# Kernel optimization log

Hardware: AMD Instinct MI355X
Metric: run time of the kernel (lower is better)

The kernel has to match this reference:

```python
import jax, jax.numpy as jnp
import numpy as np


def _init(key, shape, fan_in):
    return jax.random.normal(key, shape, jnp.float32) * (1.0 / np.sqrt(fan_in))


def setup_inputs() -> dict:
    key = jax.random.key(0)
    ks = jax.random.split(key, 12)
    b, n, vd, ad, sd, hd = 32, 2048, 512, 128, 128, 64
    return {
        'vfeat': jax.random.normal(ks[0], (b, n, vd), jnp.float32),
        'afeat': jax.random.normal(ks[1], (b, n, ad), jnp.float32),
        'vfc_w': _init(ks[2], (ad, vd), vd), 'vfc_b': jnp.zeros((ad,), jnp.float32),
        'afc_w': _init(ks[3], (ad, ad), ad), 'afc_b': jnp.zeros((ad,), jnp.float32),
        'am_v_w': _init(ks[4], (sd, sd), sd), 'am_v_b': jnp.zeros((sd,), jnp.float32),
        'am_a_w': _init(ks[5], (sd, sd), sd), 'am_a_b': jnp.zeros((sd,), jnp.float32),
        'am_o_w': _init(ks[6], (1, sd), sd), 'am_o_b': jnp.zeros((1,), jnp.float32),
        'V_w': _init(ks[7], (hd, sd), sd), 'V_b': jnp.zeros((hd,), jnp.float32),
        'W_w': _init(ks[8], (1, hd), hd), 'W_b': jnp.zeros((1,), jnp.float32),
        'cls_w': _init(ks[9], (2, sd), sd), 'cls_b': jnp.zeros((2,), jnp.float32),
    }


def reference(vfeat, afeat, vfc_w, vfc_b, afc_w, afc_b,
              am_v_w, am_v_b, am_a_w, am_a_b, am_o_w, am_o_b,
              V_w, V_b, W_w, W_b, cls_w, cls_b):
    relu = jax.nn.relu
    # vfc / afc projections (dropout is identity in eval mode)
    vo1 = relu(jnp.einsum('bnd,kd->bnk', vfeat, vfc_w) + vfc_b)  # (b,n,128)
    ax = relu(jnp.einsum('bnd,kd->bnk', afeat, afc_w) + afc_b)   # (b,n,128)
    # AM(128): additive gated cross-modal attention: out = sigmoid(Wo tanh(Wv v + Wa a)) * a
    h = jnp.tanh(jnp.einsum('bnk,jk->bnj', vo1, am_v_w) + am_v_b
                 + jnp.einsum('bnk,jk->bnj', ax, am_a_w) + am_a_b)
    att = jax.nn.sigmoid(jnp.einsum('bnj,oj->bno', h, am_o_w) + am_o_b)  # (b,n,1)
    ffeat = att * ax + vo1  # attfeat + vo1, (b,n,128)
    # NOTE: original uses self.V for BOTH f_v and f_u (source bug kept)
    f_v = relu(jnp.einsum('bnk,hk->bnh', ffeat, V_w) + V_b)  # (b,n,64)
    f_u = f_v
    # W is affine with no nonlinearity on (fv_i + fu_j), so
    # W(fv_i + fu_j) = w.fv_i + w.fu_j + b  -- exact rank-1 decomposition
    s_v = f_v @ W_w[0]  # (b,n)
    s_u = f_u @ W_w[0]  # (b,n)
    pair = s_v[:, :, None] + s_u[:, None, :] + W_b[0]  # (b,n_i,n_j)
    p = jax.nn.softmax(pair, axis=1)  # F.softmax(scores, 0) per bag: over i
    scores = p.mean(axis=2)  # mean over j -> (b,n)
    # eval mode: training-only softmax over dim 2 skipped
    zfeat = jnp.einsum('bn,bnk->bk', scores, ffeat)  # (b,128)
    logits = zfeat @ cls_w.T + cls_b  # (b,2)
    return scores, logits
```

## Files before the change

kernel.cpp:

```cpp
#include <hip/hip_runtime.h>
#include <cstddef>
#include <cstdint>


typedef __attribute__((ext_vector_type(8))) short short8;
typedef __attribute__((ext_vector_type(4))) float float4v;

#define MFMA16(a, b, c) __builtin_amdgcn_mfma_f32_16x16x32_bf16((a), (b), (c), 0, 0, 0)

__device__ __forceinline__ unsigned short f2bf(float f) {
    union { float f; unsigned u; } v; v.f = f;
    unsigned r = (v.u + 0x7fffu + ((v.u >> 16) & 1u)) >> 16;
    return (unsigned short)r;
}
__device__ __forceinline__ float bf2f(unsigned short h) {
    union { unsigned u; float f; } v; v.u = ((unsigned)h) << 16;
    return v.f;
}
__device__ __forceinline__ float bf2f_s(short h) { return bf2f((unsigned short)h); }

__device__ __forceinline__ void bfsplit(float x, short& h, short& l) {
    union { float f; unsigned u; } v; v.f = x;
    h = (short)(v.u >> 16);
    union { unsigned u; float f; } hv; hv.u = v.u & 0xffff0000u;
    union { float f; unsigned u; } lv; lv.f = x - hv.f;
    l = (short)(lv.u >> 16);
}

__device__ __forceinline__ float tanh_fast(float x) {
    float e = __builtin_exp2f(x * 2.885390081777927f);
    return 1.f - 2.f / (e + 1.f);
}
__device__ __forceinline__ float sigmoid_fast(float x) {
    return 1.f / (1.f + __builtin_exp2f(-x * 1.4426950408889634f));
}

__device__ __forceinline__ void gload_lds16(const void* g, void* l) {
#if __has_builtin(__builtin_amdgcn_global_load_lds)
    __builtin_amdgcn_global_load_lds(
        (const __attribute__((address_space(1))) unsigned int*)g,
        (__attribute__((address_space(3))) unsigned int*)l, 16, 0, 0);
#else
    *(uint4*)l = *(const uint4*)g;
#endif
}

__global__ __launch_bounds__(256)
void prep(const float* __restrict__ vfc_w, const float* __restrict__ afc_w,
          const float* __restrict__ am_v_w, const float* __restrict__ am_a_w,
          const float* __restrict__ V_w,
          unsigned short* __restrict__ W1h, unsigned short* __restrict__ W1l,
          unsigned short* __restrict__ W1bh, unsigned short* __restrict__ W1bl,
          unsigned short* __restrict__ W2v, unsigned short* __restrict__ W2a,
          unsigned short* __restrict__ W3)
{
    int t = blockIdx.x * 256 + threadIdx.x;
    if (t < 65536) {
        int j = t & 7, lane = (t >> 3) & 63, ks = (t >> 9) & 15, nf = (t >> 13) & 7;
        int n = (lane & 15) + 16 * nf, k = ks * 32 + (lane >> 4) * 8 + j;
        float x = vfc_w[n * 512 + k];
        unsigned short h = f2bf(x);
        W1h[t] = h; W1l[t] = f2bf(x - bf2f(h));
    } else if (t < 81920) {
        int u = t - 65536;
        int j = u & 7, lane = (u >> 3) & 63, ks = (u >> 9) & 3, nf = (u >> 11) & 7;
        int n = (lane & 15) + 16 * nf, k = ks * 32 + (lane >> 4) * 8 + j;
        float x = afc_w[n * 128 + k];
        unsigned short h = f2bf(x);
        W1bh[u] = h; W1bl[u] = f2bf(x - bf2f(h));
    } else if (t < 98304) {
        int u = t - 81920;
        int j = u & 7, lane = (u >> 3) & 63, ks = (u >> 9) & 3, nf = (u >> 11) & 7;
        int n = (lane & 15) + 16 * nf, k = ks * 32 + (lane >> 4) * 8 + j;
        W2v[u] = f2bf(am_v_w[n * 128 + k]);
    } else if (t < 114688) {
        int u = t - 98304;
        int j = u & 7, lane = (u >> 3) & 63, ks = (u >> 9) & 3, nf = (u >> 11) & 7;
        int n = (lane & 15) + 16 * nf, k = ks * 32 + (lane >> 4) * 8 + j;
        W2a[u] = f2bf(am_a_w[n * 128 + k]);
    } else if (t < 122880) {
        int u = t - 114688;
        int j = u & 7, lane = (u >> 3) & 63, ks = (u >> 9) & 3, nf = (u >> 11) & 3;
        int n = (lane & 15) + 16 * nf, k = ks * 32 + (lane >> 4) * 8 + j;
        W3[u] = f2bf(V_w[n * 128 + k]);
    }
}

__global__ __launch_bounds__(256, 3)
void milA(const float* __restrict__ vfeat, const float* __restrict__ afeat,
          const float* __restrict__ vfc_b, const float* __restrict__ afc_b,
          const float* __restrict__ am_v_b, const float* __restrict__ am_a_b,
          const float* __restrict__ am_o_w, const float* __restrict__ am_o_b,
          const float* __restrict__ V_b, const float* __restrict__ W_w,
          const unsigned short* __restrict__ W1h, const unsigned short* __restrict__ W1l,
          const unsigned short* __restrict__ W1bh, const unsigned short* __restrict__ W1bl,
          const unsigned short* __restrict__ W2v, const unsigned short* __restrict__ W2a,
          const unsigned short* __restrict__ W3,
          float* __restrict__ ffeat_out, float* __restrict__ s_out)
{
    __shared__ __align__(16) unsigned short vo1s[8192];
    __shared__ __align__(16) unsigned short axs[8192];
    __shared__ __align__(16) unsigned short bstage[8192];

    const int tid = threadIdx.x;
    const int lane = tid & 63, wid = tid >> 6;
    const int lr = lane & 15, lg = lane >> 4;
    const int row0 = blockIdx.x * 64 + wid * 16;

    float4v acc1[8];
#pragma unroll
    for (int nf = 0; nf < 8; ++nf)
#pragma unroll
        for (int i = 0; i < 4; ++i) acc1[nf][i] = 0.f;

    {
        const float* ap = vfeat + (size_t)(row0 + lr) * 512 + lg * 8;
        float4 a0[2], a1[2], a2[2];
        a0[0] = *(const float4*)(ap);      a0[1] = *(const float4*)(ap + 4);
        a1[0] = *(const float4*)(ap + 32); a1[1] = *(const float4*)(ap + 36);

        for (int ks = 0; ks < 16; ++ks) {
            __syncthreads();
#pragma unroll
            for (int i = 0; i < 4; ++i) {
                const int idx = wid * 4 + i;
                const unsigned short* src = (idx < 8)
                    ? W1h + (size_t)(idx * 16 + ks) * 512
                    : W1l + (size_t)((idx - 8) * 16 + ks) * 512;
                gload_lds16(src + (size_t)lane * 8, &bstage[idx * 512 + lane * 8]);
            }
            __syncthreads();

            if (ks < 14) {
                a2[0] = *(const float4*)(ap + (ks + 2) * 32);
                a2[1] = *(const float4*)(ap + (ks + 2) * 32 + 4);
            }
            short8 ah, al;
            {
                const float xs[8] = {a0[0].x, a0[0].y, a0[0].z, a0[0].w,
                                     a0[1].x, a0[1].y, a0[1].z, a0[1].w};
#pragma unroll
                for (int j = 0; j < 8; ++j) {
                    short h, l; bfsplit(xs[j], h, l);
                    ah[j] = h; al[j] = l;
                }
            }
#pragma unroll
            for (int nf = 0; nf < 8; ++nf) {
                const short8 bh = *(const short8*)&bstage[nf * 512 + lane * 8];
                const short8 bl = *(const short8*)&bstage[4096 + nf * 512 + lane * 8];
                acc1[nf] = MFMA16(ah, bh, acc1[nf]);
                acc1[nf] = MFMA16(ah, bl, acc1[nf]);
                acc1[nf] = MFMA16(al, bh, acc1[nf]);
            }
            a0[0] = a1[0]; a0[1] = a1[1];
            a1[0] = a2[0]; a1[1] = a2[1];
        }
    }
#pragma unroll
    for (int nf = 0; nf < 8; ++nf) {
        const float bb = vfc_b[lr + 16 * nf];
#pragma unroll
        for (int r = 0; r < 4; ++r) {
            float v = fmaxf(acc1[nf][r] + bb, 0.f);
            acc1[nf][r] = v;
            const int row = lg * 4 + r;
            const int col = lr + 16 * nf;
            vo1s[wid * 2048 + row * 128 + (col ^ ((row & 7) << 3))] = f2bf(v);
        }
    }

    float4v acc1b[8];
#pragma unroll
    for (int nf = 0; nf < 8; ++nf)
#pragma unroll
        for (int i = 0; i < 4; ++i) acc1b[nf][i] = 0.f;

    {
        const float* ap = afeat + (size_t)(row0 + lr) * 128 + lg * 8;
        float4 a0[2], a1[2], a2[2];
        a0[0] = *(const float4*)(ap);      a0[1] = *(const float4*)(ap + 4);
        a1[0] = *(const float4*)(ap + 32); a1[1] = *(const float4*)(ap + 36);

        for (int ks = 0; ks < 4; ++ks) {
            __syncthreads();
#pragma unroll
            for (int i = 0; i < 4; ++i) {
                const int idx = wid * 4 + i;
                const unsigned short* src = (idx < 8)
                    ? W1bh + (size_t)(idx * 4 + ks) * 512
                    : W1bl + (size_t)((idx - 8) * 4 + ks) * 512;
                gload_lds16(src + (size_t)lane * 8, &bstage[idx * 512 + lane * 8]);
            }
            __syncthreads();

            if (ks < 2) {
                a2[0] = *(const float4*)(ap + (ks + 2) * 32);
                a2[1] = *(const float4*)(ap + (ks + 2) * 32 + 4);
            }
            short8 ah, al;
            {
                const float xs[8] = {a0[0].x, a0[0].y, a0[0].z, a0[0].w,
                                     a0[1].x, a0[1].y, a0[1].z, a0[1].w};
#pragma unroll
                for (int j = 0; j < 8; ++j) {
                    short h, l; bfsplit(xs[j], h, l);
                    ah[j] = h; al[j] = l;
                }
            }
#pragma unroll
            for (int nf = 0; nf < 8; ++nf) {
                const short8 bh = *(const short8*)&bstage[nf * 512 + lane * 8];
                const short8 bl = *(const short8*)&bstage[4096 + nf * 512 + lane * 8];
                acc1b[nf] = MFMA16(ah, bh, acc1b[nf]);
                acc1b[nf] = MFMA16(ah, bl, acc1b[nf]);
                acc1b[nf] = MFMA16(al, bh, acc1b[nf]);
            }
            a0[0] = a1[0]; a0[1] = a1[1];
            a1[0] = a2[0]; a1[1] = a2[1];
        }
    }
#pragma unroll
    for (int nf = 0; nf < 8; ++nf) {
        const float bb = afc_b[lr + 16 * nf];
#pragma unroll
        for (int r = 0; r < 4; ++r) {
            float v = fmaxf(acc1b[nf][r] + bb, 0.f);
            acc1b[nf][r] = v;
            const int row = lg * 4 + r;
            const int col = lr + 16 * nf;
            axs[wid * 2048 + row * 128 + (col ^ ((row & 7) << 3))] = f2bf(v);
        }
    }

    float4v acc2[8];
#pragma unroll
    for (int nf = 0; nf < 8; ++nf)
#pragma unroll
        for (int i = 0; i < 4; ++i) acc2[nf][i] = 0.f;

    for (int ks = 0; ks < 4; ++ks) {
        __syncthreads();
#pragma unroll
        for (int i = 0; i < 4; ++i) {
            const int idx = wid * 4 + i;
            const unsigned short* src = (idx < 8)
                ? W2v + (size_t)(idx * 4 + ks) * 512
                : W2a + (size_t)((idx - 8) * 4 + ks) * 512;
            gload_lds16(src + (size_t)lane * 8, &bstage[idx * 512 + lane * 8]);
        }
        __syncthreads();
        const int rdoff = (ks * 32 + lg * 8) ^ ((lr & 7) << 3);
        const short8 a2v = *(const short8*)&vo1s[wid * 2048 + lr * 128 + rdoff];
        const short8 a2a = *(const short8*)&axs[wid * 2048 + lr * 128 + rdoff];
#pragma unroll
        for (int nf = 0; nf < 8; ++nf) {
            const short8 bv = *(const short8*)&bstage[nf * 512 + lane * 8];
            const short8 ba = *(const short8*)&bstage[4096 + nf * 512 + lane * 8];
            acc2[nf] = MFMA16(a2v, bv, acc2[nf]);
            acc2[nf] = MFMA16(a2a, ba, acc2[nf]);
        }
    }

    __syncthreads();
#pragma unroll
    for (int i = 0; i < 4; ++i) {
        const int idx = wid * 4 + i;
        gload_lds16(W3 + (size_t)idx * 512 + lane * 8, &bstage[idx * 512 + lane * 8]);
    }

    float attc[4];
    {
        float bias2[8], wo[8];
#pragma unroll
        for (int nf = 0; nf < 8; ++nf) {
            const int c = lr + 16 * nf;
            bias2[nf] = am_v_b[c] + am_a_b[c];
            wo[nf] = am_o_w[c];
        }
        const float ob = am_o_b[0];
#pragma unroll
        for (int r = 0; r < 4; ++r) {
            float p = 0.f;
#pragma unroll
            for (int nf = 0; nf < 8; ++nf)
                p += tanh_fast(acc2[nf][r] + bias2[nf]) * wo[nf];
            p += __shfl_xor(p, 1);
            p += __shfl_xor(p, 2);
            p += __shfl_xor(p, 4);
            p += __shfl_xor(p, 8);
            attc[r] = sigmoid_fast(p + ob);
        }
    }

#pragma unroll
    for (int nf = 0; nf < 8; ++nf)
#pragma unroll
        for (int r = 0; r < 4; ++r)
            ffeat_out[(size_t)(row0 + lg * 4 + r) * 128 + lr + 16 * nf] =
                attc[r] * acc1b[nf][r] + acc1[nf][r];

    float attv;
    {
        const int srcl = (lr >> 2) << 4;
        const float b0 = __shfl(attc[0], srcl);
        const float b1 = __shfl(attc[1], srcl);
        const float b2 = __shfl(attc[2], srcl);
        const float b3 = __shfl(attc[3], srcl);
        attv = (lr & 2) ? ((lr & 1) ? b3 : b2) : ((lr & 1) ? b1 : b0);
    }

    __syncthreads();

    float4v acc3[4];
#pragma unroll
    for (int nf = 0; nf < 4; ++nf)
#pragma unroll
        for (int i = 0; i < 4; ++i) acc3[nf][i] = 0.f;

#pragma unroll
    for (int ks = 0; ks < 4; ++ks) {
        const int rdoff = (ks * 32 + lg * 8) ^ ((lr & 7) << 3);
        const short8 x8 = *(const short8*)&axs[wid * 2048 + lr * 128 + rdoff];
        const short8 v8 = *(const short8*)&vo1s[wid * 2048 + lr * 128 + rdoff];
        short8 a3;
#pragma unroll
        for (int j = 0; j < 8; ++j) {
            float f = attv * bf2f_s(x8[j]) + bf2f_s(v8[j]);
            a3[j] = (short)f2bf(f);
        }
#pragma unroll
        for (int nf = 0; nf < 4; ++nf) {
            const short8 b = *(const short8*)&bstage[(nf * 4 + ks) * 512 + lane * 8];
            acc3[nf] = MFMA16(a3, b, acc3[nf]);
        }
    }

    {
        float vb3[4], ww3[4];
#pragma unroll
        for (int nf = 0; nf < 4; ++nf) {
            const int c = lr + 16 * nf;
            vb3[nf] = V_b[c];
            ww3[nf] = W_w[c];
        }
#pragma unroll
        for (int r = 0; r < 4; ++r) {
            float q = 0.f;
#pragma unroll
            for (int nf = 0; nf < 4; ++nf)
                q += fmaxf(acc3[nf][r] + vb3[nf], 0.f) * ww3[nf];
            q += __shfl_xor(q, 1);
            q += __shfl_xor(q, 2);
            q += __shfl_xor(q, 4);
            q += __shfl_xor(q, 8);
            if (lr == 0) s_out[row0 + lg * 4 + r] = q;
        }
    }
}

__device__ __forceinline__ float wred_sum(float v) {
#pragma unroll
    for (int m = 32; m >= 1; m >>= 1) v += __shfl_xor(v, m);
    return v;
}
__device__ __forceinline__ float wred_max(float v) {
#pragma unroll
    for (int m = 32; m >= 1; m >>= 1) v = fmaxf(v, __shfl_xor(v, m));
    return v;
}

__global__ __launch_bounds__(256)
void milB1(const float* __restrict__ s_in, float* __restrict__ scores_out)
{
    __shared__ float red[4];
    const int t = threadIdx.x, b = blockIdx.x, w = t >> 6;
    const float* sb = s_in + (size_t)b * 2048;

    float v[8];
#pragma unroll
    for (int q = 0; q < 8; ++q) v[q] = sb[q * 256 + t];
    float m = v[0];
#pragma unroll
    for (int q = 1; q < 8; ++q) m = fmaxf(m, v[q]);
    m = wred_max(m);
    if ((t & 63) == 0) red[w] = m;
    __syncthreads();
    const float bm = fmaxf(fmaxf(red[0], red[1]), fmaxf(red[2], red[3]));

    float e[8], sum = 0.f;
#pragma unroll
    for (int q = 0; q < 8; ++q) { e[q] = expf(v[q] - bm); sum += e[q]; }
    sum = wred_sum(sum);
    __syncthreads();
    if ((t & 63) == 0) red[w] = sum;
    __syncthreads();
    const float inv = 1.f / (red[0] + red[1] + red[2] + red[3]);
#pragma unroll
    for (int q = 0; q < 8; ++q)
        scores_out[(size_t)b * 2048 + q * 256 + t] = e[q] * inv;
}

__global__ __launch_bounds__(256)
void milB2(const float* __restrict__ scores, const float* __restrict__ ffeat,
           float* __restrict__ parts)
{
    __shared__ float sh[256];
    __shared__ float zbuf[256];
    const int t = threadIdx.x;
    const int b = blockIdx.x >> 3, part = blockIdx.x & 7;
    const int col = t & 127, half = t >> 7;

    sh[t] = scores[(size_t)b * 2048 + part * 256 + t];
    __syncthreads();

    const float* fb = ffeat + ((size_t)(b * 2048 + part * 256 + half * 128)) * 128 + col;
    const float* sp = sh + half * 128;
    float z = 0.f;
#pragma unroll 8
    for (int nn = 0; nn < 128; ++nn) z += sp[nn] * fb[(size_t)nn * 128];
    zbuf[t] = z;
    __syncthreads();
    if (t < 128) parts[((size_t)(b * 8 + part)) * 128 + t] = zbuf[t] + zbuf[t + 128];
}

__global__ __launch_bounds__(128)
void milB3(const float* __restrict__ parts, const float* __restrict__ cls_w,
           const float* __restrict__ cls_b, float* __restrict__ logits)
{
    __shared__ float zfs[128];
    const int t = threadIdx.x, b = blockIdx.x;
    float zf = 0.f;
#pragma unroll
    for (int p = 0; p < 8; ++p) zf += parts[((size_t)(b * 8 + p)) * 128 + t];
    zfs[t] = zf;
    __syncthreads();
    const int o = t >> 6, c = t & 63;
    float q = zfs[c] * cls_w[o * 128 + c] + zfs[c + 64] * cls_w[o * 128 + c + 64];
    q = wred_sum(q);
    if (c == 0) logits[b * 2 + o] = q + cls_b[o];
}

extern "C" void kernel_launch(void* const* d_in, const int* in_sizes, int n_in,
                              void* d_out, int out_size, void* d_ws, size_t ws_size,
                              hipStream_t stream)
{
    (void)in_sizes; (void)n_in; (void)out_size; (void)ws_size;
    const float* vfeat  = (const float*)d_in[0];
    const float* afeat  = (const float*)d_in[1];
    const float* vfc_w  = (const float*)d_in[2];
    const float* vfc_b  = (const float*)d_in[3];
    const float* afc_w  = (const float*)d_in[4];
    const float* afc_b  = (const float*)d_in[5];
    const float* am_v_w = (const float*)d_in[6];
    const float* am_v_b = (const float*)d_in[7];
    const float* am_a_w = (const float*)d_in[8];
    const float* am_a_b = (const float*)d_in[9];
    const float* am_o_w = (const float*)d_in[10];
    const float* am_o_b = (const float*)d_in[11];
    const float* V_w    = (const float*)d_in[12];
    const float* V_b    = (const float*)d_in[13];
    const float* W_w    = (const float*)d_in[14];
    const float* cls_w  = (const float*)d_in[16];
    const float* cls_b  = (const float*)d_in[17];

    float* scores = (float*)d_out;
    float* logits = (float*)d_out + 32 * 2048;

    char* ws = (char*)d_ws;
    float* ffeat_ws = (float*)ws;
    float* s_ws     = (float*)(ws + 33554432);
    float* parts_ws = (float*)(ws + 33816576);
    unsigned short* W1h  = (unsigned short*)(ws + 33947648);
    unsigned short* W1l  = W1h + 65536;
    unsigned short* W1bh = W1l + 65536;
    unsigned short* W1bl = W1bh + 16384;
    unsigned short* W2v  = W1bl + 16384;
    unsigned short* W2a  = W2v + 16384;
    unsigned short* W3   = W2a + 16384;

    prep<<<480, 256, 0, stream>>>(vfc_w, afc_w, am_v_w, am_a_w, V_w,
                                  W1h, W1l, W1bh, W1bl, W2v, W2a, W3);
    milA<<<1024, 256, 0, stream>>>(vfeat, afeat, vfc_b, afc_b, am_v_b, am_a_b,
                                   am_o_w, am_o_b, V_b, W_w,
                                   W1h, W1l, W1bh, W1bl, W2v, W2a, W3,
                                   ffeat_ws, s_ws);
    milB1<<<32, 256, 0, stream>>>(s_ws, scores);
    milB2<<<256, 256, 0, stream>>>(scores, ffeat_ws, parts_ws);
    milB3<<<32, 128, 0, stream>>>(parts_ws, cls_w, cls_b, logits);
}
```

Baseline: 88.82 us.

## Stage two K-slices of weights per barrier pair and prefetch afeat early

Doubles the shared-memory weight staging buffer so each sync round loads two K-steps of the weight tiles, halving the number of barrier pairs in the vfc, afc and AM GEMM loops. The activation prefetch now covers a 64-wide K chunk, and the first afeat chunk is loaded during the last vfeat step so the afc stage starts without waiting on it. LDS use grows and launch bounds drop from 3 to 2 blocks per SM, which cuts occupancy available for hiding latency.

New measurement: 84.81 us. -4.5%, faster.

```diff
diff --git a/kernel.cpp b/kernel.cpp
--- a/kernel.cpp
+++ b/kernel.cpp
@@ -86,7 +86,7 @@
     }
 }
 
-__global__ __launch_bounds__(256, 3)
+__global__ __launch_bounds__(256, 2)
 void milA(const float* __restrict__ vfeat, const float* __restrict__ afeat,
           const float* __restrict__ vfc_b, const float* __restrict__ afc_b,
           const float* __restrict__ am_v_b, const float* __restrict__ am_a_b,
@@ -98,47 +98,58 @@
           const unsigned short* __restrict__ W3,
           float* __restrict__ ffeat_out, float* __restrict__ s_out)
 {
+    __shared__ __align__(16) unsigned short bstage[16384];
     __shared__ __align__(16) unsigned short vo1s[8192];
     __shared__ __align__(16) unsigned short axs[8192];
-    __shared__ __align__(16) unsigned short bstage[8192];
 
     const int tid = threadIdx.x;
     const int lane = tid & 63, wid = tid >> 6;
     const int lr = lane & 15, lg = lane >> 4;
     const int row0 = blockIdx.x * 64 + wid * 16;
 
+    const float* ap  = vfeat + (size_t)(row0 + lr) * 512 + lg * 8;
+    const float* apb = afeat + (size_t)(row0 + lr) * 128 + lg * 8;
+
     float4v acc1[8];
 #pragma unroll
     for (int nf = 0; nf < 8; ++nf)
 #pragma unroll
         for (int i = 0; i < 4; ++i) acc1[nf][i] = 0.f;
 
-    {
-        const float* ap = vfeat + (size_t)(row0 + lr) * 512 + lg * 8;
-        float4 a0[2], a1[2], a2[2];
-        a0[0] = *(const float4*)(ap);      a0[1] = *(const float4*)(ap + 4);
-        a1[0] = *(const float4*)(ap + 32); a1[1] = *(const float4*)(ap + 36);
-
-        for (int ks = 0; ks < 16; ++ks) {
-            __syncthreads();
-#pragma unroll
-            for (int i = 0; i < 4; ++i) {
-                const int idx = wid * 4 + i;
-                const unsigned short* src = (idx < 8)
-                    ? W1h + (size_t)(idx * 16 + ks) * 512
-                    : W1l + (size_t)((idx - 8) * 16 + ks) * 512;
-                gload_lds16(src + (size_t)lane * 8, &bstage[idx * 512 + lane * 8]);
-            }
-            __syncthreads();
-
-            if (ks < 14) {
-                a2[0] = *(const float4*)(ap + (ks + 2) * 32);
-                a2[1] = *(const float4*)(ap + (ks + 2) * 32 + 4);
-            }
+    float4 acur[4], anxt[4];
+#pragma unroll
+    for (int q = 0; q < 4; ++q)
+        acur[q] = *(const float4*)(ap + (q >> 1) * 32 + (q & 1) * 4);
+
+    for (int s = 0; s < 8; ++s) {
+        __syncthreads();
+#pragma unroll
+        for (int i = 0; i < 8; ++i) {
+            const int f = wid * 8 + i;
+            const int ksl = f >> 4, rest = f & 15, isl = rest >> 3, nf = rest & 7;
+            const unsigned short* src = (isl ? W1l : W1h)
+                + (size_t)(nf * 16 + (s * 2 + ksl)) * 512 + (size_t)lane * 8;
+            gload_lds16(src, &bstage[f * 512 + lane * 8]);
+        }
+        __syncthreads();
+
+        if (s < 7) {
+            const float* apn = ap + (s + 1) * 64;
+#pragma unroll
+            for (int q = 0; q < 4; ++q)
+                anxt[q] = *(const float4*)(apn + (q >> 1) * 32 + (q & 1) * 4);
+        } else {
+#pragma unroll
+            for (int q = 0; q < 4; ++q)
+                anxt[q] = *(const float4*)(apb + (q >> 1) * 32 + (q & 1) * 4);
+        }
+
+#pragma unroll
+        for (int ksl = 0; ksl < 2; ++ksl) {
             short8 ah, al;
             {
-                const float xs[8] = {a0[0].x, a0[0].y, a0[0].z, a0[0].w,
-                                     a0[1].x, a0[1].y, a0[1].z, a0[1].w};
+                const float4 x0 = acur[ksl * 2], x1 = acur[ksl * 2 + 1];
+                const float xs[8] = {x0.x, x0.y, x0.z, x0.w, x1.x, x1.y, x1.z, x1.w};
 #pragma unroll
                 for (int j = 0; j < 8; ++j) {
                     short h, l; bfsplit(xs[j], h, l);
@@ -147,15 +158,15 @@
             }
 #pragma unroll
             for (int nf = 0; nf < 8; ++nf) {
-                const short8 bh = *(const short8*)&bstage[nf * 512 + lane * 8];
-                const short8 bl = *(const short8*)&bstage[4096 + nf * 512 + lane * 8];
+                const short8 bh = *(const short8*)&bstage[(ksl * 16 + nf) * 512 + lane * 8];
+                const short8 bl = *(const short8*)&bstage[(ksl * 16 + 8 + nf) * 512 + lane * 8];
                 acc1[nf] = MFMA16(ah, bh, acc1[nf]);
                 acc1[nf] = MFMA16(ah, bl, acc1[nf]);
                 acc1[nf] = MFMA16(al, bh, acc1[nf]);
             }
-            a0[0] = a1[0]; a0[1] = a1[1];
-            a1[0] = a2[0]; a1[1] = a2[1];
-        }
+        }
+#pragma unroll
+        for (int q = 0; q < 4; ++q) acur[q] = anxt[q];
     }
 #pragma unroll
     for (int nf = 0; nf < 8; ++nf) {
@@ -176,32 +187,31 @@
 #pragma unroll
         for (int i = 0; i < 4; ++i) acc1b[nf][i] = 0.f;
 
-    {
-        const float* ap = afeat + (size_t)(row0 + lr) * 128 + lg * 8;
-        float4 a0[2], a1[2], a2[2];
-        a0[0] = *(const float4*)(ap);      a0[1] = *(const float4*)(ap + 4);
-        a1[0] = *(const float4*)(ap + 32); a1[1] = *(const float4*)(ap + 36);
-
-        for (int ks = 0; ks < 4; ++ks) {
-            __syncthreads();
-#pragma unroll
-            for (int i = 0; i < 4; ++i) {
-                const int idx = wid * 4 + i;
-                const unsigned short* src = (idx < 8)
-                    ? W1bh + (size_t)(idx * 4 + ks) * 512
-                    : W1bl + (size_t)((idx - 8) * 4 + ks) * 512;
-                gload_lds16(src + (size_t)lane * 8, &bstage[idx * 512 + lane * 8]);
-            }
-            __syncthreads();
-
-            if (ks < 2) {
-                a2[0] = *(const float4*)(ap + (ks + 2) * 32);
-                a2[1] = *(const float4*)(ap + (ks + 2) * 32 + 4);
-            }
+    for (int s = 0; s < 2; ++s) {
+        __syncthreads();
+#pragma unroll
+        for (int i = 0; i < 8; ++i) {
+            const int f = wid * 8 + i;
+            const int ksl = f >> 4, rest = f & 15, isl = rest >> 3, nf = rest & 7;
+            const unsigned short* src = (isl ? W1bl : W1bh)
+                + (size_t)(nf * 4 + (s * 2 + ksl)) * 512 + (size_t)lane * 8;
+            gload_lds16(src, &bstage[f * 512 + lane * 8]);
+        }
+        __syncthreads();
+
+        if (s < 1) {
+            const float* apn = apb + 64;
+#pragma unroll
+            for (int q = 0; q < 4; ++q)
+                anxt[q] = *(const float4*)(apn + (q >> 1) * 32 + (q & 1) * 4);
+        }
+
+#pragma unroll
+        for (int ksl = 0; ksl < 2; ++ksl) {
             short8 ah, al;
             {
-                const float xs[8] = {a0[0].x, a0[0].y, a0[0].z, a0[0].w,
-                                     a0[1].x, a0[1].y, a0[1].z, a0[1].w};
+                const float4 x0 = acur[ksl * 2], x1 = acur[ksl * 2 + 1];
+                const float xs[8] = {x0.x, x0.y, x0.z, x0.w, x1.x, x1.y, x1.z, x1.w};
 #pragma unroll
                 for (int j = 0; j < 8; ++j) {
                     short h, l; bfsplit(xs[j], h, l);
@@ -210,15 +220,15 @@
             }
 #pragma unroll
             for (int nf = 0; nf < 8; ++nf) {
-                const short8 bh = *(const short8*)&bstage[nf * 512 + lane * 8];
-                const short8 bl = *(const short8*)&bstage[4096 + nf * 512 + lane * 8];
+                const short8 bh = *(const short8*)&bstage[(ksl * 16 + nf) * 512 + lane * 8];
+                const short8 bl = *(const short8*)&bstage[(ksl * 16 + 8 + nf) * 512 + lane * 8];
                 acc1b[nf] = MFMA16(ah, bh, acc1b[nf]);
                 acc1b[nf] = MFMA16(ah, bl, acc1b[nf]);
                 acc1b[nf] = MFMA16(al, bh, acc1b[nf]);
             }
-            a0[0] = a1[0]; a0[1] = a1[1];
-            a1[0] = a2[0]; a1[1] = a2[1];
-        }
+        }
+#pragma unroll
+        for (int q = 0; q < 4; ++q) acur[q] = anxt[q];
     }
 #pragma unroll
     for (int nf = 0; nf < 8; ++nf) {
@@ -239,34 +249,39 @@
 #pragma unroll
         for (int i = 0; i < 4; ++i) acc2[nf][i] = 0.f;
 
-    for (int ks = 0; ks < 4; ++ks) {
+    for (int s = 0; s < 2; ++s) {
         __syncthreads();
 #pragma unroll
-        for (int i = 0; i < 4; ++i) {
-            const int idx = wid * 4 + i;
-            const unsigned short* src = (idx < 8)
-                ? W2v + (size_t)(idx * 4 + ks) * 512
-                : W2a + (size_t)((idx - 8) * 4 + ks) * 512;
-            gload_lds16(src + (size_t)lane * 8, &bstage[idx * 512 + lane * 8]);
+        for (int i = 0; i < 8; ++i) {
+            const int f = wid * 8 + i;
+            const int ksl = f >> 4, rest = f & 15, isa = rest >> 3, nf = rest & 7;
+            const unsigned short* src = (isa ? W2a : W2v)
+                + (size_t)(nf * 4 + (s * 2 + ksl)) * 512 + (size_t)lane * 8;
+            gload_lds16(src, &bstage[f * 512 + lane * 8]);
         }
         __syncthreads();
-        const int rdoff = (ks * 32 + lg * 8) ^ ((lr & 7) << 3);
-        const short8 a2v = *(const short8*)&vo1s[wid * 2048 + lr * 128 + rdoff];
-        const short8 a2a = *(const short8*)&axs[wid * 2048 + lr * 128 + rdoff];
-#pragma unroll
-        for (int nf = 0; nf < 8; ++nf) {
-            const short8 bv = *(const short8*)&bstage[nf * 512 + lane * 8];
-            const short8 ba = *(const short8*)&bstage[4096 + nf * 512 + lane * 8];
-            acc2[nf] = MFMA16(a2v, bv, acc2[nf]);
-            acc2[nf] = MFMA16(a2a, ba, acc2[nf]);
+
+#pragma unroll
+        for (int ksl = 0; ksl < 2; ++ksl) {
+            const int ks = s * 2 + ksl;
+            const int rdoff = (ks * 32 + lg * 8) ^ ((lr & 7) << 3);
+            const short8 a2v = *(const short8*)&vo1s[wid * 2048 + lr * 128 + rdoff];
+            const short8 a2a = *(const short8*)&axs[wid * 2048 + lr * 128 + rdoff];
+#pragma unroll
+            for (int nf = 0; nf < 8; ++nf) {
+                const short8 bv = *(const short8*)&bstage[(ksl * 16 + nf) * 512 + lane * 8];
+                const short8 ba = *(const short8*)&bstage[(ksl * 16 + 8 + nf) * 512 + lane * 8];
+                acc2[nf] = MFMA16(a2v, bv, acc2[nf]);
+                acc2[nf] = MFMA16(a2a, ba, acc2[nf]);
+            }
         }
     }
 
     __syncthreads();
 #pragma unroll
     for (int i = 0; i < 4; ++i) {
-        const int idx = wid * 4 + i;
-        gload_lds16(W3 + (size_t)idx * 512 + lane * 8, &bstage[idx * 512 + lane * 8]);
+        const int f = wid * 4 + i;
+        gload_lds16(W3 + (size_t)f * 512 + lane * 8, &bstage[f * 512 + lane * 8]);
     }
 
     float attc[4];
```

## Double-buffer weight staging in LDS and prefetch next tile across GEMM phases

Applied to the files above, without the earlier changes.

Replaces the single LDS weight staging buffer, which needed two barriers per k-step, with a ping-pong double buffer. The next tile's global-to-LDS load is issued before the current tile's MFMAs, using explicit vmcnt waits and one barrier per step. The pipeline now carries across the vfc, afc, AM and V phases, so each phase's first weights are prefetched during the previous phase. LDS use grows and launch bounds drop from 3 to 2 blocks per CU, which trades occupancy for overlap.

New measurement: 87.64 us. About the same (-1.3%).

```diff
diff --git a/kernel.cpp b/kernel.cpp
--- a/kernel.cpp
+++ b/kernel.cpp
@@ -7,6 +7,8 @@
 typedef __attribute__((ext_vector_type(4))) float float4v;
 
 #define MFMA16(a, b, c) __builtin_amdgcn_mfma_f32_16x16x32_bf16((a), (b), (c), 0, 0, 0)
+#define VMCNT(n) asm volatile("s_waitcnt vmcnt(" #n ")" ::: "memory")
+#define BARRIER() __builtin_amdgcn_s_barrier()
 
 __device__ __forceinline__ unsigned short f2bf(float f) {
     union { float f; unsigned u; } v; v.f = f;
@@ -86,7 +88,7 @@
     }
 }
 
-__global__ __launch_bounds__(256, 3)
+__global__ __launch_bounds__(256, 2)
 void milA(const float* __restrict__ vfeat, const float* __restrict__ afeat,
           const float* __restrict__ vfc_b, const float* __restrict__ afc_b,
           const float* __restrict__ am_v_b, const float* __restrict__ am_a_b,
@@ -98,64 +100,89 @@
           const unsigned short* __restrict__ W3,
           float* __restrict__ ffeat_out, float* __restrict__ s_out)
 {
+    __shared__ __align__(16) unsigned short bstage[2][8192];
     __shared__ __align__(16) unsigned short vo1s[8192];
     __shared__ __align__(16) unsigned short axs[8192];
-    __shared__ __align__(16) unsigned short bstage[8192];
 
     const int tid = threadIdx.x;
     const int lane = tid & 63, wid = tid >> 6;
     const int lr = lane & 15, lg = lane >> 4;
     const int row0 = blockIdx.x * 64 + wid * 16;
 
+    const float* apv = vfeat + (size_t)(row0 + lr) * 512 + lg * 8;
+    const float* apa = afeat + (size_t)(row0 + lr) * 128 + lg * 8;
+
+    auto stage16 = [&](const unsigned short* th, const unsigned short* tl,
+                       int nks, int ks, int buf) {
+#pragma unroll
+        for (int i = 0; i < 4; ++i) {
+            const int f = wid * 4 + i;
+            const int nf = f & 7;
+            const unsigned short* src = ((f >> 3) ? tl : th)
+                + ((size_t)(nf * nks + ks)) * 512 + (size_t)lane * 8;
+            gload_lds16(src, &bstage[buf][f * 512 + lane * 8]);
+        }
+    };
+    auto stage_w3 = [&](int buf) {
+#pragma unroll
+        for (int i = 0; i < 4; ++i) {
+            const int f = wid * 4 + i;
+            gload_lds16(W3 + (size_t)f * 512 + lane * 8,
+                        &bstage[buf][f * 512 + lane * 8]);
+        }
+    };
+
+    float4 a0[2], a1[2], a2[2];
+    auto loadA = [&](float4 (&a)[2], const float* ap, int ks) {
+        a[0] = *(const float4*)(ap + ks * 32);
+        a[1] = *(const float4*)(ap + ks * 32 + 4);
+    };
+    auto rotA = [&]() {
+        a0[0] = a1[0]; a0[1] = a1[1];
+        a1[0] = a2[0]; a1[1] = a2[1];
+    };
+    auto convA = [&](short8& ah, short8& al) {
+        const float xs[8] = {a0[0].x, a0[0].y, a0[0].z, a0[0].w,
+                             a0[1].x, a0[1].y, a0[1].z, a0[1].w};
+#pragma unroll
+        for (int j = 0; j < 8; ++j) {
+            short h, l; bfsplit(xs[j], h, l);
+            ah[j] = h; al[j] = l;
+        }
+    };
+
     float4v acc1[8];
 #pragma unroll
     for (int nf = 0; nf < 8; ++nf)
 #pragma unroll
         for (int i = 0; i < 4; ++i) acc1[nf][i] = 0.f;
 
-    {
-        const float* ap = vfeat + (size_t)(row0 + lr) * 512 + lg * 8;
-        float4 a0[2], a1[2], a2[2];
-        a0[0] = *(const float4*)(ap);      a0[1] = *(const float4*)(ap + 4);
-        a1[0] = *(const float4*)(ap + 32); a1[1] = *(const float4*)(ap + 36);
-
-        for (int ks = 0; ks < 16; ++ks) {
-            __syncthreads();
-#pragma unroll
-            for (int i = 0; i < 4; ++i) {
-                const int idx = wid * 4 + i;
-                const unsigned short* src = (idx < 8)
-                    ? W1h + (size_t)(idx * 16 + ks) * 512
-                    : W1l + (size_t)((idx - 8) * 16 + ks) * 512;
-                gload_lds16(src + (size_t)lane * 8, &bstage[idx * 512 + lane * 8]);
-            }
-            __syncthreads();
-
-            if (ks < 14) {
-                a2[0] = *(const float4*)(ap + (ks + 2) * 32);
-                a2[1] = *(const float4*)(ap + (ks + 2) * 32 + 4);
-            }
-            short8 ah, al;
-            {
-                const float xs[8] = {a0[0].x, a0[0].y, a0[0].z, a0[0].w,
-                                     a0[1].x, a0[1].y, a0[1].z, a0[1].w};
-#pragma unroll
-                for (int j = 0; j < 8; ++j) {
-                    short h, l; bfsplit(xs[j], h, l);
-                    ah[j] = h; al[j] = l;
-                }
-            }
-#pragma unroll
-            for (int nf = 0; nf < 8; ++nf) {
-                const short8 bh = *(const short8*)&bstage[nf * 512 + lane * 8];
-                const short8 bl = *(const short8*)&bstage[4096 + nf * 512 + lane * 8];
-                acc1[nf] = MFMA16(ah, bh, acc1[nf]);
-                acc1[nf] = MFMA16(ah, bl, acc1[nf]);
-                acc1[nf] = MFMA16(al, bh, acc1[nf]);
-            }
-            a0[0] = a1[0]; a0[1] = a1[1];
-            a1[0] = a2[0]; a1[1] = a2[1];
-        }
+    stage16(W1h, W1l, 16, 0, 0);
+    loadA(a0, apv, 0);
+    loadA(a1, apv, 1);
+    VMCNT(2);
+    BARRIER();
+
+    for (int ks = 0; ks < 16; ++ks) {
+        const int cur = ks & 1;
+        if (ks < 15) stage16(W1h, W1l, 16, ks + 1, cur ^ 1);
+        else         stage16(W1bh, W1bl, 4, 0, cur ^ 1);
+        if (ks < 14) loadA(a2, apv, ks + 2);
+        else         loadA(a2, apa, ks - 14);
+
+        short8 ah, al;
+        convA(ah, al);
+#pragma unroll
+        for (int nf = 0; nf < 8; ++nf) {
+            const short8 bh = *(const short8*)&bstage[cur][nf * 512 + lane * 8];
+            const short8 bl = *(const short8*)&bstage[cur][(8 + nf) * 512 + lane * 8];
+            acc1[nf] = MFMA16(ah, bh, acc1[nf]);
+            acc1[nf] = MFMA16(ah, bl, acc1[nf]);
+            acc1[nf] = MFMA16(al, bh, acc1[nf]);
+        }
+        rotA();
+        VMCNT(2);
+        BARRIER();
     }
 #pragma unroll
     for (int nf = 0; nf < 8; ++nf) {
@@ -176,49 +203,25 @@
 #pragma unroll
         for (int i = 0; i < 4; ++i) acc1b[nf][i] = 0.f;
 
-    {
-        const float* ap = afeat + (size_t)(row0 + lr) * 128 + lg * 8;
-        float4 a0[2], a1[2], a2[2];
-        a0[0] = *(const float4*)(ap);      a0[1] = *(const float4*)(ap + 4);
-        a1[0] = *(const float4*)(ap + 32); a1[1] = *(const float4*)(ap + 36);
-
-        for (int ks = 0; ks < 4; ++ks) {
-            __syncthreads();
-#pragma unroll
-            for (int i = 0; i < 4; ++i) {
-                const int idx = wid * 4 + i;
-                const unsigned short* src = (idx < 8)
-                    ? W1bh + (size_t)(idx * 4 + ks) * 512
-                    : W1bl + (size_t)((idx - 8) * 4 + ks) * 512;
-                gload_lds16(src + (size_t)lane * 8, &bstage[idx * 512 + lane * 8]);
-            }
-            __syncthreads();
-
-            if (ks < 2) {
-                a2[0] = *(const float4*)(ap + (ks + 2) * 32);
-                a2[1] = *(const float4*)(ap + (ks + 2) * 32 + 4);
-            }
-            short8 ah, al;
-            {
-                const float xs[8] = {a0[0].x, a0[0].y, a0[0].z, a0[0].w,
-                                     a0[1].x, a0[1].y, a0[1].z, a0[1].w};
-#pragma unroll
-                for (int j = 0; j < 8; ++j) {
-                    short h, l; bfsplit(xs[j], h, l);
-                    ah[j] = h; al[j] = l;
-                }
-            }
-#pragma unroll
-            for (int nf = 0; nf < 8; ++nf) {
-                const short8 bh = *(const short8*)&bstage[nf * 512 + lane * 8];
-                const short8 bl = *(const short8*)&bstage[4096 + nf * 512 + lane * 8];
-                acc1b[nf] = MFMA16(ah, bh, acc1b[nf]);
-                acc1b[nf] = MFMA16(ah, bl, acc1b[nf]);
-                acc1b[nf] = MFMA16(al, bh, acc1b[nf]);
-            }
-            a0[0] = a1[0]; a0[1] = a1[1];
-            a1[0] = a2[0]; a1[1] = a2[1];
-        }
+    for (int ks = 0; ks < 4; ++ks) {
+        const int cur = ks & 1;
+        if (ks < 3) stage16(W1bh, W1bl, 4, ks + 1, cur ^ 1);
+        else        stage16(W2v, W2a, 4, 0, cur ^ 1);
+        if (ks < 2) loadA(a2, apa, ks + 2);
+
+        short8 ah, al;
+        convA(ah, al);
+#pragma unroll
+        for (int nf = 0; nf < 8; ++nf) {
+            const short8 bh = *(const short8*)&bstage[cur][nf * 512 + lane * 8];
+            const short8 bl = *(const short8*)&bstage[cur][(8 + nf) * 512 + lane * 8];
+            acc1b[nf] = MFMA16(ah, bh, acc1b[nf]);
+            acc1b[nf] = MFMA16(ah, bl, acc1b[nf]);
+            acc1b[nf] = MFMA16(al, bh, acc1b[nf]);
+        }
+        rotA();
+        if (ks < 2) { VMCNT(2); } else { VMCNT(0); }
+        BARRIER();
     }
 #pragma unroll
     for (int nf = 0; nf < 8; ++nf) {
@@ -240,33 +243,22 @@
         for (int i = 0; i < 4; ++i) acc2[nf][i] = 0.f;
 
     for (int ks = 0; ks < 4; ++ks) {
-        __syncthreads();
-#pragma unroll
-        for (int i = 0; i < 4; ++i) {
-            const int idx = wid * 4 + i;
-            const unsigned short* src = (idx < 8)
-                ? W2v + (size_t)(idx * 4 + ks) * 512
-                : W2a + (size_t)((idx - 8) * 4 + ks) * 512;
-            gload_lds16(src + (size_t)lane * 8, &bstage[idx * 512 + lane * 8]);
-        }
-        __syncthreads();
+        const int cur = ks & 1;
+        if (ks < 3) stage16(W2v, W2a, 4, ks + 1, cur ^ 1);
+        else        stage_w3(cur ^ 1);
+
         const int rdoff = (ks * 32 + lg * 8) ^ ((lr & 7) << 3);
         const short8 a2v = *(const short8*)&vo1s[wid * 2048 + lr * 128 + rdoff];
         const short8 a2a = *(const short8*)&axs[wid * 2048 + lr * 128 + rdoff];
 #pragma unroll
         for (int nf = 0; nf < 8; ++nf) {
-            const short8 bv = *(const short8*)&bstage[nf * 512 + lane * 8];
-            const short8 ba = *(const short8*)&bstage[4096 + nf * 512 + lane * 8];
+            const short8 bv = *(const short8*)&bstage[cur][nf * 512 + lane * 8];
+            const short8 ba = *(const short8*)&bstage[cur][(8 + nf) * 512 + lane * 8];
             acc2[nf] = MFMA16(a2v, bv, acc2[nf]);
             acc2[nf] = MFMA16(a2a, ba, acc2[nf]);
         }
-    }
-
-    __syncthreads();
-#pragma unroll
-    for (int i = 0; i < 4; ++i) {
-        const int idx = wid * 4 + i;
-        gload_lds16(W3 + (size_t)idx * 512 + lane * 8, &bstage[idx * 512 + lane * 8]);
+        VMCNT(0);
+        BARRIER();
     }
 
     float attc[4];
@@ -310,8 +302,6 @@
         attv = (lr & 2) ? ((lr & 1) ? b3 : b2) : ((lr & 1) ? b1 : b0);
     }
 
-    __syncthreads();
-
     float4v acc3[4];
 #pragma unroll
     for (int nf = 0; nf < 4; ++nf)
@@ -331,7 +321,7 @@
         }
 #pragma unroll
         for (int nf = 0; nf < 4; ++nf) {
-            const short8 b = *(const short8*)&bstage[(nf * 4 + ks) * 512 + lane * 8];
+            const short8 b = *(const short8*)&bstage[0][(nf * 4 + ks) * 512 + lane * 8];
             acc3[nf] = MFMA16(a3, b, acc3[nf]);
         }
     }
```

## Split vfeat projection into separate register-resident-weight kernel

Applied to the files above, without the earlier changes.

Moves the 512-wide vfeat projection out of the fused kernel into a new kernel, milA1. Each wave keeps its slice of the bf16 hi/lo weights in registers and computes 64 rows by 16 columns, so there is no LDS staging and no per-k-step block barriers. The ReLU result is written to the ffeat workspace in fp32. The second kernel reads it back, runs the afeat and attention path, and overwrites the same buffer in place with ffeat. This trades the barrier-heavy staged GEMM for an extra 32 MB write and read of intermediates plus one more launch.

New measurement: 188.3 us. +112.0%, slower.

```diff
diff --git a/kernel.cpp b/kernel.cpp
--- a/kernel.cpp
+++ b/kernel.cpp
@@ -86,17 +86,91 @@
     }
 }
 
+__global__ __launch_bounds__(256, 2)
+void milA1(const float* __restrict__ vfeat, const float* __restrict__ vfc_b,
+           const unsigned short* __restrict__ W1h,
+           const unsigned short* __restrict__ W1l,
+           float* __restrict__ vo1f)
+{
+    const int tid = threadIdx.x;
+    const int lane = tid & 63, wid = tid >> 6;
+    const int lr = lane & 15, lg = lane >> 4;
+    const int rowtile = blockIdx.x >> 2, colq = blockIdx.x & 3;
+    const int rg = wid >> 1, cg = wid & 1;
+    const int nf = colq * 2 + cg;
+    const int rbase = rowtile * 128 + rg * 64;
+
+    short8 bh[16], bl[16];
+#pragma unroll
+    for (int ks = 0; ks < 16; ++ks) {
+        bh[ks] = *(const short8*)(W1h + ((size_t)(nf * 16 + ks) * 64 + lane) * 8);
+        bl[ks] = *(const short8*)(W1l + ((size_t)(nf * 16 + ks) * 64 + lane) * 8);
+    }
+
+    float4v acc[4];
+#pragma unroll
+    for (int rf = 0; rf < 4; ++rf)
+#pragma unroll
+        for (int i = 0; i < 4; ++i) acc[rf][i] = 0.f;
+
+    const float* ap = vfeat + (size_t)(rbase + lr) * 512 + lg * 8;
+
+    float4 cur[8], nxt[8];
+#pragma unroll
+    for (int rf = 0; rf < 4; ++rf) {
+        cur[rf * 2]     = *(const float4*)(ap + (size_t)rf * 16 * 512);
+        cur[rf * 2 + 1] = *(const float4*)(ap + (size_t)rf * 16 * 512 + 4);
+    }
+
+#pragma unroll
+    for (int ks = 0; ks < 16; ++ks) {
+        if (ks < 15) {
+#pragma unroll
+            for (int rf = 0; rf < 4; ++rf) {
+                nxt[rf * 2]     = *(const float4*)(ap + (size_t)rf * 16 * 512 + (ks + 1) * 32);
+                nxt[rf * 2 + 1] = *(const float4*)(ap + (size_t)rf * 16 * 512 + (ks + 1) * 32 + 4);
+            }
+        }
+#pragma unroll
+        for (int rf = 0; rf < 4; ++rf) {
+            const float xs[8] = {cur[rf*2].x, cur[rf*2].y, cur[rf*2].z, cur[rf*2].w,
+                                 cur[rf*2+1].x, cur[rf*2+1].y, cur[rf*2+1].z, cur[rf*2+1].w};
+            short8 ah, al;
+#pragma unroll
+            for (int j = 0; j < 8; ++j) {
+                short h, l; bfsplit(xs[j], h, l);
+                ah[j] = h; al[j] = l;
+            }
+            acc[rf] = MFMA16(ah, bh[ks], acc[rf]);
+            acc[rf] = MFMA16(ah, bl[ks], acc[rf]);
+            acc[rf] = MFMA16(al, bh[ks], acc[rf]);
+        }
+        if (ks < 15) {
+#pragma unroll
+            for (int q = 0; q < 8; ++q) cur[q] = nxt[q];
+        }
+    }
+
+    const float bb = vfc_b[lr + 16 * nf];
+#pragma unroll
+    for (int rf = 0; rf < 4; ++rf)
+#pragma unroll
+        for (int r = 0; r < 4; ++r)
+            vo1f[(size_t)(rbase + rf * 16 + lg * 4 + r) * 128 + lr + 16 * nf] =
+                fmaxf(acc[rf][r] + bb, 0.f);
+}
+
 __global__ __launch_bounds__(256, 3)
-void milA(const float* __restrict__ vfeat, const float* __restrict__ afeat,
-          const float* __restrict__ vfc_b, const float* __restrict__ afc_b,
-          const float* __restrict__ am_v_b, const float* __restrict__ am_a_b,
-          const float* __restrict__ am_o_w, const float* __restrict__ am_o_b,
-          const float* __restrict__ V_b, const float* __restrict__ W_w,
-          const unsigned short* __restrict__ W1h, const unsigned short* __restrict__ W1l,
-          const unsigned short* __restrict__ W1bh, const unsigned short* __restrict__ W1bl,
-          const unsigned short* __restrict__ W2v, const unsigned short* __restrict__ W2a,
-          const unsigned short* __restrict__ W3,
-          float* __restrict__ ffeat_out, float* __restrict__ s_out)
+void milA2(const float* __restrict__ afeat,
+           const float* __restrict__ afc_b,
+           const float* __restrict__ am_v_b, const float* __restrict__ am_a_b,
+           const float* __restrict__ am_o_w, const float* __restrict__ am_o_b,
+           const float* __restrict__ V_b, const float* __restrict__ W_w,
+           const unsigned short* __restrict__ W1bh, const unsigned short* __restrict__ W1bl,
+           const unsigned short* __restrict__ W2v, const unsigned short* __restrict__ W2a,
+           const unsigned short* __restrict__ W3,
+           float* vof,
+           float* __restrict__ s_out)
 {
     __shared__ __align__(16) unsigned short vo1s[8192];
     __shared__ __align__(16) unsigned short axs[8192];
@@ -107,68 +181,17 @@
     const int lr = lane & 15, lg = lane >> 4;
     const int row0 = blockIdx.x * 64 + wid * 16;
 
-    float4v acc1[8];
+    float vo1r[8][4];
 #pragma unroll
     for (int nf = 0; nf < 8; ++nf)
 #pragma unroll
-        for (int i = 0; i < 4; ++i) acc1[nf][i] = 0.f;
-
-    {
-        const float* ap = vfeat + (size_t)(row0 + lr) * 512 + lg * 8;
-        float4 a0[2], a1[2], a2[2];
-        a0[0] = *(const float4*)(ap);      a0[1] = *(const float4*)(ap + 4);
-        a1[0] = *(const float4*)(ap + 32); a1[1] = *(const float4*)(ap + 36);
-
-        for (int ks = 0; ks < 16; ++ks) {
-            __syncthreads();
-#pragma unroll
-            for (int i = 0; i < 4; ++i) {
-                const int idx = wid * 4 + i;
-                const unsigned short* src = (idx < 8)
-                    ? W1h + (size_t)(idx * 16 + ks) * 512
-                    : W1l + (size_t)((idx - 8) * 16 + ks) * 512;
-                gload_lds16(src + (size_t)lane * 8, &bstage[idx * 512 + lane * 8]);
-            }
-            __syncthreads();
-
-            if (ks < 14) {
-                a2[0] = *(const float4*)(ap + (ks + 2) * 32);
-                a2[1] = *(const float4*)(ap + (ks + 2) * 32 + 4);
-            }
-            short8 ah, al;
-            {
-                const float xs[8] = {a0[0].x, a0[0].y, a0[0].z, a0[0].w,
-                                     a0[1].x, a0[1].y, a0[1].z, a0[1].w};
-#pragma unroll
-                for (int j = 0; j < 8; ++j) {
-                    short h, l; bfsplit(xs[j], h, l);
-                    ah[j] = h; al[j] = l;
-                }
-            }
-#pragma unroll
-            for (int nf = 0; nf < 8; ++nf) {
-                const short8 bh = *(const short8*)&bstage[nf * 512 + lane * 8];
-                const short8 bl = *(const short8*)&bstage[4096 + nf * 512 + lane * 8];
-                acc1[nf] = MFMA16(ah, bh, acc1[nf]);
-                acc1[nf] = MFMA16(ah, bl, acc1[nf]);
-                acc1[nf] = MFMA16(al, bh, acc1[nf]);
-            }
-            a0[0] = a1[0]; a0[1] = a1[1];
-            a1[0] = a2[0]; a1[1] = a2[1];
-        }
-    }
-#pragma unroll
-    for (int nf = 0; nf < 8; ++nf) {
-        const float bb = vfc_b[lr + 16 * nf];
-#pragma unroll
         for (int r = 0; r < 4; ++r) {
-            float v = fmaxf(acc1[nf][r] + bb, 0.f);
-            acc1[nf][r] = v;
+            const float v = vof[(size_t)(row0 + lg * 4 + r) * 128 + lr + 16 * nf];
+            vo1r[nf][r] = v;
             const int row = lg * 4 + r;
             const int col = lr + 16 * nf;
             vo1s[wid * 2048 + row * 128 + (col ^ ((row & 7) << 3))] = f2bf(v);
         }
-    }
 
     float4v acc1b[8];
 #pragma unroll
@@ -186,11 +209,11 @@
             __syncthreads();
 #pragma unroll
             for (int i = 0; i < 4; ++i) {
-                const int idx = wid * 4 + i;
-                const unsigned short* src = (idx < 8)
-                    ? W1bh + (size_t)(idx * 4 + ks) * 512
-                    : W1bl + (size_t)((idx - 8) * 4 + ks) * 512;
-                gload_lds16(src + (size_t)lane * 8, &bstage[idx * 512 + lane * 8]);
+                const int f = wid * 4 + i;
+                const int nf = f & 7;
+                const unsigned short* src = ((f >> 3) ? W1bl : W1bh)
+                    + (size_t)(nf * 4 + ks) * 512 + (size_t)lane * 8;
+                gload_lds16(src, &bstage[f * 512 + lane * 8]);
             }
             __syncthreads();
 
@@ -211,7 +234,7 @@
 #pragma unroll
             for (int nf = 0; nf < 8; ++nf) {
                 const short8 bh = *(const short8*)&bstage[nf * 512 + lane * 8];
-                const short8 bl = *(const short8*)&bstage[4096 + nf * 512 + lane * 8];
+                const short8 bl = *(const short8*)&bstage[(8 + nf) * 512 + lane * 8];
                 acc1b[nf] = MFMA16(ah, bh, acc1b[nf]);
                 acc1b[nf] = MFMA16(ah, bl, acc1b[nf]);
                 acc1b[nf] = MFMA16(al, bh, acc1b[nf]);
@@ -243,11 +266,11 @@
         __syncthreads();
 #pragma unroll
         for (int i = 0; i < 4; ++i) {
-            const int idx = wid * 4 + i;
-            const unsigned short* src = (idx < 8)
-                ? W2v + (size_t)(idx * 4 + ks) * 512
-                : W2a + (size_t)((idx - 8) * 4 + ks) * 512;
-            gload_lds16(src + (size_t)lane * 8, &bstage[idx * 512 + lane * 8]);
+            const int f = wid * 4 + i;
+            const int nf = f & 7;
+            const unsigned short* src = ((f >> 3) ? W2a : W2v)
+                + (size_t)(nf * 4 + ks) * 512 + (size_t)lane * 8;
+            gload_lds16(src, &bstage[f * 512 + lane * 8]);
         }
         __syncthreads();
         const int rdoff = (ks * 32 + lg * 8) ^ ((lr & 7) << 3);
@@ -256,7 +279,7 @@
 #pragma unroll
         for (int nf = 0; nf < 8; ++nf) {
             const short8 bv = *(const short8*)&bstage[nf * 512 + lane * 8];
-            const short8 ba = *(const short8*)&bstage[4096 + nf * 512 + lane * 8];
+            const short8 ba = *(const short8*)&bstage[(8 + nf) * 512 + lane * 8];
             acc2[nf] = MFMA16(a2v, bv, acc2[nf]);
             acc2[nf] = MFMA16(a2a, ba, acc2[nf]);
         }
@@ -265,8 +288,8 @@
     __syncthreads();
 #pragma unroll
     for (int i = 0; i < 4; ++i) {
-        const int idx = wid * 4 + i;
-        gload_lds16(W3 + (size_t)idx * 512 + lane * 8, &bstage[idx * 512 + lane * 8]);
+        const int f = wid * 4 + i;
+        gload_lds16(W3 + (size_t)f * 512 + lane * 8, &bstage[f * 512 + lane * 8]);
     }
 
     float attc[4];
@@ -297,8 +320,8 @@
     for (int nf = 0; nf < 8; ++nf)
 #pragma unroll
         for (int r = 0; r < 4; ++r)
-            ffeat_out[(size_t)(row0 + lg * 4 + r) * 128 + lr + 16 * nf] =
-                attc[r] * acc1b[nf][r] + acc1[nf][r];
+            vof[(size_t)(row0 + lg * 4 + r) * 128 + lr + 16 * nf] =
+                attc[r] * acc1b[nf][r] + vo1r[nf][r];
 
     float attv;
     {
@@ -468,7 +491,7 @@
     float* logits = (float*)d_out + 32 * 2048;
 
     char* ws = (char*)d_ws;
-    float* ffeat_ws = (float*)ws;
+    float* vof      = (float*)ws;
     float* s_ws     = (float*)(ws + 33554432);
     float* parts_ws = (float*)(ws + 33816576);
     unsigned short* W1h  = (unsigned short*)(ws + 33947648);
@@ -481,11 +504,12 @@
 
     prep<<<480, 256, 0, stream>>>(vfc_w, afc_w, am_v_w, am_a_w, V_w,
                                   W1h, W1l, W1bh, W1bl, W2v, W2a, W3);
-    milA<<<1024, 256, 0, stream>>>(vfeat, afeat, vfc_b, afc_b, am_v_b, am_a_b,
-                                   am_o_w, am_o_b, V_b, W_w,
-                                   W1h, W1l, W1bh, W1bl, W2v, W2a, W3,
-                                   ffeat_ws, s_ws);
+    milA1<<<2048, 256, 0, stream>>>(vfeat, vfc_b, W1h, W1l, vof);
+    milA2<<<1024, 256, 0, stream>>>(afeat, afc_b, am_v_b, am_a_b,
+                                    am_o_w, am_o_b, V_b, W_w,
+                                    W1bh, W1bl, W2v, W2a, W3,
+                                    vof, s_ws);
     milB1<<<32, 256, 0, stream>>>(s_ws, scores);
-    milB2<<<256, 256, 0, stream>>>(scores, ffeat_ws, parts_ws);
+    milB2<<<256, 256, 0, stream>>>(scores, vof, parts_ws);
     milB3<<<32, 128, 0, stream>>>(parts_ws, cls_w, cls_b, logits);
 }
```
